# Performance work log

Measured on AMD Instinct MI355X. Metric: run time of the kernel, lower is better.

The kernel has to match this reference:

```python
import jax, jax.numpy as jnp
import numpy as np

B, L, D, H, FF, K = 2, 2048, 512, 16, 2048, 5
HD = D // H
EPS = 1e-5


def _ln(x, g, b):
    m = jnp.mean(x, axis=-1, keepdims=True)
    v = jnp.var(x, axis=-1, keepdims=True)
    return (x - m) / jnp.sqrt(v + EPS) * g + b


def _rope_table(seq_len, hd):
    pos = jnp.arange(seq_len, dtype=jnp.float32)
    inv = 1.0 / (10000.0 ** (jnp.arange(0, hd, 2, dtype=jnp.float32) / hd))
    ang = pos[:, None] * inv[None, :]            # [L, hd/2]
    return jnp.concatenate([jnp.cos(ang), jnp.sin(ang)], axis=-1)  # [L, hd]


def setup_inputs() -> dict:
    key = jax.random.key(0)
    ks = jax.random.split(key, 32)
    w = lambda k, shape: jax.random.normal(k, shape, jnp.float32) * 0.02
    z = lambda n: jnp.zeros((n,), jnp.float32)
    o = lambda n: jnp.ones((n,), jnp.float32)
    return {
        'src': jax.random.normal(ks[0], (B, L, D), jnp.float32),
        'Wq': w(ks[1], (D, D)), 'bq': z(D),
        'Wk': w(ks[2], (D, D)), 'bk': z(D),
        'Wv': w(ks[3], (D, D)), 'bv': z(D),
        'Wo': w(ks[4], (D, D)), 'bo': z(D),
        'ln_g': o(D), 'ln_b': z(D),
        'pw1_w': w(ks[5], (2 * D, D)), 'pw1_b': z(2 * D),
        'dw_w': w(ks[6], (D, 1, K)), 'dw_b': z(D),
        'bn_g': o(D), 'bn_b': z(D),
        'pw2_w': w(ks[7], (D, D)), 'pw2_b': z(D),
        'proj_w': w(ks[8], (L, L)), 'proj_b': z(L),
        'proj2_w': w(ks[9], (D, D)), 'proj2_b': z(D),
        'W1': w(ks[10], (FF, D)), 'b1': z(FF),
        'W2': w(ks[11], (D, FF)), 'b2': z(D),
        'n1_g': o(D), 'n1_b': z(D),
        'n2_g': o(D), 'n2_b': z(D),
    }


def reference(src, Wq, bq, Wk, bk, Wv, bv, Wo, bo, ln_g, ln_b,
              pw1_w, pw1_b, dw_w, dw_b, bn_g, bn_b, pw2_w, pw2_b,
              proj_w, proj_b, proj2_w, proj2_b, W1, b1, W2, b2,
              n1_g, n1_b, n2_g, n2_b):
    scale = HD ** -0.5
    pe = _rope_table(L, HD)
    c, s = pe[:, ::2], pe[:, 1::2]   # faithful to apply_RoPE's interleaved slicing of [cos|sin]

    def rope(x):  # x: [B,H,L,hd]
        xe, xo = x[..., ::2], x[..., 1::2]
        return jnp.concatenate([xe * c - xo * s, xe * s + xo * c], axis=-1)

    q = (src @ Wq.T + bq).reshape(B, L, H, HD).transpose(0, 2, 1, 3)
    k = (src @ Wk.T + bk).reshape(B, L, H, HD).transpose(0, 2, 1, 3)
    v = (src @ Wv.T + bv).reshape(B, L, H, HD).transpose(0, 2, 1, 3)
    q, k = rope(q), rope(k)

    slopes = jnp.asarray(2.0 ** (-(2.0 ** (-(np.log2(H) - 3.0))) * np.arange(H)), jnp.float32)
    idx = jnp.arange(L)
    dist = jnp.clip(idx[:, None] - idx[None, :], 0, None).astype(jnp.float32)
    alibi = slopes[:, None, None] * dist  # [H,L,L]

    scores = jnp.einsum('bhld,bhmd->bhlm', q, k) * scale + alibi[None]
    attn = jax.nn.softmax(scores, axis=-1)
    ctx = jnp.einsum('bhlm,bhmd->bhld', attn, v).transpose(0, 2, 1, 3).reshape(B, L, D)
    attn_out = ctx @ Wo.T + bo

    x0 = src + _ln(attn_out, n1_g, n1_b)

    # depthwise conformer conv block (stride=1, residual downsample = identity)
    x = _ln(x0, ln_g, ln_b)
    x = x @ pw1_w.T + pw1_b                      # [B,L,2D]
    a, g = x[..., :D], x[..., D:]
    x = a * jax.nn.sigmoid(g)                    # GLU
    x = x.transpose(0, 2, 1)                     # [B,D,L]
    x = jax.lax.conv_general_dilated(x, dw_w, (1,), [(K // 2, K // 2)],
                                     dimension_numbers=('NCH', 'OIH', 'NCH'),
                                     feature_group_count=D) + dw_b[None, :, None]
    x = x * (bn_g / jnp.sqrt(1.0 + EPS))[None, :, None] + bn_b[None, :, None]  # BN eval (mu=0, var=1)
    x = x * jnp.clip(x + 3.0, 0.0, 6.0) / 6.0    # hardswish
    conv = x.transpose(0, 2, 1) @ pw2_w.T + pw2_b + x0

    # seq-dim projection branch
    p = jnp.einsum('bld,ml->bmd', x0, proj_w) + proj_b[None, :, None]
    p = p @ proj2_w.T + proj2_b

    y = p + conv
    ff = jax.nn.gelu(y @ W1.T + b1, approximate=False) @ W2.T + b2
    return _ln(y + ff, n2_g, n2_b)
```

## Files before the change

kernel.cpp:

```cpp
#include <hip/hip_runtime.h>
#include <math.h>

#define B_ 2
#define L_ 2048
#define D_ 512
#define H_ 16
#define HD_ 32
#define FF_ 2048
#define BL_ 4096
#define EPS_ 1e-5f

typedef unsigned short ushort;
typedef unsigned int uint;
typedef __attribute__((ext_vector_type(8))) short bf16x8;
typedef __attribute__((ext_vector_type(4))) float f32x4;
typedef __attribute__((ext_vector_type(4))) uint u32x4;

__device__ __forceinline__ ushort bf16r(float f) {
  uint u = __float_as_uint(f);
  uint r = (u + 0x7FFFu + ((u >> 16) & 1u)) >> 16;
  return (ushort)r;
}
__device__ __forceinline__ float bf2f(uint u) { return __uint_as_float(u << 16); }

__device__ __forceinline__ float wsum(float v) {
#pragma unroll
  for (int o = 32; o; o >>= 1) v += __shfl_xor(v, o);
  return v;
}

__device__ __forceinline__ float gelu_fast(float x) {
  float t = x + 0.044715f * x * x * x;
  float e = exp2f(fminf(2.302118131f * t, 80.f));
  return x * e / (1.f + e);
}

__device__ __forceinline__ void gload16(const void* g, void* l) {
  __builtin_amdgcn_global_load_lds(
      (const __attribute__((address_space(1))) void*)g,
      (__attribute__((address_space(3))) void*)l, 16, 0, 0);
}

template <int TMv, int TNv, int EPI, int BROW, int GELU, int RES, int OUTF, int OUTB, int SPK>
__global__ __launch_bounds__(256, 2) void gemm_bf_k(
    const ushort* __restrict__ A, const ushort* __restrict__ W,
    const float* __restrict__ bias, const float* __restrict__ res,
    float* __restrict__ Cf, ushort* __restrict__ Cb,
    const int M, const int N, const int Kd, const long sW, const long sC,
    const int ldC,
    const float* __restrict__ tab, ushort* __restrict__ Qb,
    ushort* __restrict__ Kb, ushort* __restrict__ Vb) {
  constexpr int MF = (TMv == 128) ? 4 : ((TNv == 128) ? 4 : 2);
  constexpr int NF = (TNv == 128) ? ((TMv == 128) ? 4 : 2) : 2;
  __shared__ __align__(16) ushort As[TMv * 64];
  __shared__ __align__(16) ushort Ws[TNv * 64];
  const int tid = threadIdx.x;
  const int wid = tid >> 6, lane = tid & 63;
  const int lane15 = lane & 15, lgrp = lane >> 4;
  const int rowoff = (TMv == 128) ? (wid >> 1) * 64
                                  : ((TNv == 64) ? (wid >> 1) * 32 : 0);
  const int wnoff = (TMv == 128) ? (wid & 1) * 64
                                 : ((TNv == 128) ? wid * 32 : (wid & 1) * 32);
  const int bm = blockIdx.y * TMv, bn = blockIdx.x * TNv;
  const int z = blockIdx.z;
  const int lda = SPK ? (Kd << 1) : Kd;
  const int kh = SPK ? (z & 1) : 0;
  const int zb = SPK ? (z >> 1) : z;
  const ushort* Az = A + (size_t)kh * Kd;
  const ushort* Wz = W + (size_t)zb * sW + (size_t)kh * Kd;

  f32x4 acc[MF][NF];
#pragma unroll
  for (int i = 0; i < MF; ++i)
#pragma unroll
    for (int j = 0; j < NF; ++j) acc[i][j] = (f32x4){0.f, 0.f, 0.f, 0.f};

  for (int k0 = 0; k0 < Kd; k0 += 64) {
    __syncthreads();
#pragma unroll
    for (int i = 0; i < TMv / 32; ++i) {
      const int cb = i * 256 + wid * 64;
      const int chunk = cb + lane;
      const int ml = chunk >> 3;
      const int c16 = (chunk & 7) ^ (ml & 7);
      gload16(Az + (size_t)(bm + ml) * lda + k0 + c16 * 8, &As[(size_t)cb * 8]);
    }
#pragma unroll
    for (int i = 0; i < TNv / 32; ++i) {
      const int cb = i * 256 + wid * 64;
      const int chunk = cb + lane;
      const int ml = chunk >> 3;
      const int c16 = (chunk & 7) ^ (ml & 7);
      gload16(Wz + (size_t)(bn + ml) * lda + k0 + c16 * 8, &Ws[(size_t)cb * 8]);
    }
    __syncthreads();

    bf16x8 af[2][MF], wf[2][NF];
#pragma unroll
    for (int kk = 0; kk < 2; ++kk) {
#pragma unroll
      for (int f = 0; f < MF; ++f) {
        const int ma = rowoff + f * 16 + lane15;
        const int ca = (kk * 4 + lgrp) ^ (ma & 7);
        af[kk][f] = *(const bf16x8*)&As[ma * 64 + ca * 8];
      }
#pragma unroll
      for (int f = 0; f < NF; ++f) {
        const int nb = wnoff + f * 16 + lane15;
        const int cw = (kk * 4 + lgrp) ^ (nb & 7);
        wf[kk][f] = *(const bf16x8*)&Ws[nb * 64 + cw * 8];
      }
    }
#pragma unroll
    for (int kk = 0; kk < 2; ++kk)
#pragma unroll
      for (int fm = 0; fm < MF; ++fm)
#pragma unroll
        for (int fn = 0; fn < NF; ++fn)
          acc[fm][fn] = __builtin_amdgcn_mfma_f32_16x16x32_bf16(
              af[kk][fm], wf[kk][fn], acc[fm][fn], 0, 0, 0);
  }

#pragma unroll
  for (int fm = 0; fm < MF; ++fm) {
#pragma unroll
    for (int fn = 0; fn < NF; ++fn) {
      const int n = bn + wnoff + fn * 16 + lane15;
      float bcol = 0.f;
      if (EPI == 2) bcol = bias[(n >> 1) + (n & 1) * 512];
      else if ((EPI == 1 || !BROW) && bias) bcol = bias[n];
#pragma unroll
      for (int r = 0; r < 4; ++r) {
        const int m = bm + rowoff + fm * 16 + lgrp * 4 + r;
        float val = acc[fm][fn][r];
        if (EPI == 1) {
          val += bcol;
          float p = __shfl_xor(val, 1);
          const int l = m & 2047, b = m >> 11;
          const int h = (n >> 5) & 15;
          if (n < 1024) {
            const int ch = n & 31, i2 = ch >> 1;
            const float cv = tab[l * 32 + i2], sv = tab[l * 32 + 16 + i2];
            const float o = (ch & 1) ? (p * sv + val * cv) : (val * cv - p * sv);
            const int dcol = (ch & 1) ? 16 + i2 : i2;
            if (n < 512)
              Qb[(((size_t)(b * 16 + h)) * 2048 + l) * 32 + dcol] =
                  bf16r(o * (0.1767766952966369f * 1.4426950408889634f));
            else
              Kb[(((size_t)(b * 16 + h)) * 2048 + l) * 32 + dcol] = bf16r(o);
          } else {
            Vb[(((size_t)(b * 16 + h)) * 2048 + l) * 32 + (n & 31)] = bf16r(val);
          }
        } else if (EPI == 2) {
          val += bcol;
          float p = __shfl_xor(val, 1);
          if (!(n & 1)) {
            float glu = val / (1.f + __expf(-p));
            Cb[(size_t)m * 512 + (n >> 1)] = bf16r(glu);
          }
        } else {
          val += BROW ? (bias ? bias[m] : 0.f) : bcol;
          if (RES) val += res[(size_t)m * N + n];
          if (GELU) val = gelu_fast(val);
          const size_t o = (size_t)z * sC + (size_t)m * ldC + n;
          if (OUTF) Cf[o] = val;
          if (OUTB) Cb[o] = bf16r(val);
        }
      }
    }
  }
}

struct CvtArgs {
  const float* s[11];
  ushort* d[11];
  int n[11];
  int pm[11];
};
__global__ __launch_bounds__(256) void cvt_all_k(CvtArgs a) {
  const int seg = blockIdx.y;
  const int n = a.n[seg];
  const int i = (blockIdx.x * 256 + threadIdx.x) * 8;
  if (i >= n) return;
  const float* s = a.s[seg] + i;
  float4 x = *(const float4*)s, y = *(const float4*)(s + 4);
  bf16x8 o;
  o[0] = (short)bf16r(x.x); o[1] = (short)bf16r(x.y);
  o[2] = (short)bf16r(x.z); o[3] = (short)bf16r(x.w);
  o[4] = (short)bf16r(y.x); o[5] = (short)bf16r(y.y);
  o[6] = (short)bf16r(y.z); o[7] = (short)bf16r(y.w);
  ushort* d = a.d[seg] + i;
  const int pm = a.pm[seg];
  if (pm == 1) {
    int cc = i >> 3;
    int row = cc >> 6, off = cc & 63;
    int nrow = (row < 512) ? row * 2 : (row - 512) * 2 + 1;
    d = a.d[seg] + (((size_t)nrow << 6) + off) * 8;
  } else if (pm >= 2) {
    d = a.d[seg] + (size_t)(i >> 9) * 1024 + (i & 511) + ((pm == 3) ? 512 : 0);
  }
  *(bf16x8*)d = o;
}

__global__ void misc_k(float* __restrict__ tab, const float* __restrict__ bq,
                       const float* __restrict__ bk, const float* __restrict__ bv,
                       float* __restrict__ bqkv, const float* __restrict__ p2b,
                       const float* __restrict__ pw2b, float* __restrict__ bcat) {
  if (blockIdx.x < 128) {
    int t = blockIdx.x * 256 + threadIdx.x;
    int i = t & 15, l = t >> 4;
    float cv, sv;
    if (i < 8) {
      float inv0 = 1.0f / powf(10000.0f, (float)(2 * i) / 16.0f);
      float inv1 = 1.0f / powf(10000.0f, (float)(2 * i + 1) / 16.0f);
      cv = cosf((float)l * inv0);
      sv = cosf((float)l * inv1);
    } else {
      int ii = i - 8;
      float inv0 = 1.0f / powf(10000.0f, (float)(2 * ii) / 16.0f);
      float inv1 = 1.0f / powf(10000.0f, (float)(2 * ii + 1) / 16.0f);
      cv = sinf((float)l * inv0);
      sv = sinf((float)l * inv1);
    }
    tab[l * 32 + i] = cv;
    tab[l * 32 + 16 + i] = sv;
  } else {
    int i = threadIdx.x;
    bqkv[i] = bq[i];            bqkv[i + 256] = bq[i + 256];
    bqkv[512 + i] = bk[i];      bqkv[768 + i] = bk[i + 256];
    bqkv[1024 + i] = bv[i];     bqkv[1280 + i] = bv[i + 256];
    bcat[i] = p2b[i] + pw2b[i];
    bcat[i + 256] = p2b[i + 256] + pw2b[i + 256];
  }
}

__global__ __launch_bounds__(256) void transp_k(const float* __restrict__ x,
                                                ushort* __restrict__ xT) {
  __shared__ float t[32][33];
  const int b = blockIdx.z, l0 = blockIdx.x * 32, d0 = blockIdx.y * 32;
  const int tx = threadIdx.x & 31, ty = threadIdx.x >> 5;
#pragma unroll
  for (int i = 0; i < 4; ++i)
    t[ty + i * 8][tx] = x[((size_t)(b * L_ + l0 + ty + i * 8)) * D_ + d0 + tx];
  __syncthreads();
#pragma unroll
  for (int i = 0; i < 4; ++i)
    xT[((size_t)(b * D_ + d0 + ty + i * 8)) * L_ + l0 + tx] =
        bf16r(t[tx][ty + i * 8]);
}

__global__ __launch_bounds__(256) void cmb_proj_k(const ushort* __restrict__ p,
                                                  const float* __restrict__ biasRow,
                                                  ushort* __restrict__ cat) {
  int t = blockIdx.x * 256 + threadIdx.x;
  int n4 = t & 127;
  int m = (t >> 7) & 2047;
  int zb = t >> 18;
  size_t i0 = ((size_t)(zb * 2) * 2048 + m) * 512 + n4 * 4;
  uint2 a = *(const uint2*)&p[i0];
  uint2 b = *(const uint2*)&p[i0 + (size_t)2048 * 512];
  float bm = biasRow[m];
  float o0 = bf2f(a.x & 0xffffu) + bf2f(b.x & 0xffffu) + bm;
  float o1 = bf2f(a.x >> 16) + bf2f(b.x >> 16) + bm;
  float o2 = bf2f(a.y & 0xffffu) + bf2f(b.y & 0xffffu) + bm;
  float o3 = bf2f(a.y >> 16) + bf2f(b.y >> 16) + bm;
  uint lo = (uint)bf16r(o0) | ((uint)bf16r(o1) << 16);
  uint hi = (uint)bf16r(o2) | ((uint)bf16r(o3) << 16);
  uint2 ov = {lo, hi};
  *(uint2*)&cat[((size_t)(zb * 2048 + m)) * 1024 + n4 * 4] = ov;
}

__global__ __launch_bounds__(512, 4) void attn_mfma_k(const ushort* __restrict__ q,
                                                      const ushort* __restrict__ k,
                                                      const ushort* __restrict__ v,
                                                      ushort* __restrict__ ctx) {
  __shared__ __align__(16) ushort K_lds[4][130][8];
  __shared__ __align__(16) uint V_lds[32][68];
  const int tid = threadIdx.x;
  const int wid = tid >> 6, lane = tid & 63;
  const int s = lane >> 4, lr = lane & 15;
  const int bid = blockIdx.x;
  const int xcd = bid & 7, idx = bid >> 3;
  const int bh = xcd * 4 + (idx & 3);
  const int qt = idx >> 2;
  const int qb = qt * 128;
  const int h = bh & 15, bidx = bh >> 4;
  const float nslope = -exp2f(-0.5f * (float)h) * 1.4426950408889634f;
  const int qrow = qb + wid * 16 + lr;
  const float qgf = (float)qrow;
  const float cq = nslope * qgf;
  bf16x8 qa = *(const bf16x8*)&q[((size_t)bh * L_ + qrow) * HD_ + s * 8];

  bf16x8 vones;
#pragma unroll
  for (int i = 0; i < 8; ++i) vones[i] = (short)0x3F80;

  f32x4 acc0 = {0.f, 0.f, 0.f, 0.f}, acc1 = {0.f, 0.f, 0.f, 0.f};
  f32x4 accl = {0.f, 0.f, 0.f, 0.f};
  const ushort* kg = k + (size_t)bh * L_ * HD_;
  const ushort* vg = v + (size_t)bh * L_ * HD_;
  const int vslot = (lane & 48) + ((lane >> 1) & 3) * 4 + ((lane >> 3) & 1) * 2 + (lane & 1);
  const int kkey = tid >> 2, kslot = tid & 3;

  bf16x8 kreg;
  uint2 va, vb;
  {
    kreg = *(const bf16x8*)&kg[(size_t)kkey * HD_ + kslot * 8];
    const ushort* g0 = vg + (size_t)(2 * lane) * HD_ + wid * 4;
    va = *(const uint2*)g0;
    vb = *(const uint2*)(g0 + HD_);
  }

  for (int t0 = 0; t0 < L_; t0 += 128) {
    __syncthreads();
    *(bf16x8*)&K_lds[kslot][kkey][0] = kreg;
    V_lds[wid * 4 + 0][vslot] = __builtin_amdgcn_perm(vb.x, va.x, 0x05040100u);
    V_lds[wid * 4 + 1][vslot] = __builtin_amdgcn_perm(vb.x, va.x, 0x07060302u);
    V_lds[wid * 4 + 2][vslot] = __builtin_amdgcn_perm(vb.y, va.y, 0x05040100u);
    V_lds[wid * 4 + 3][vslot] = __builtin_amdgcn_perm(vb.y, va.y, 0x07060302u);
    if (t0 + 128 < L_) {
      kreg = *(const bf16x8*)&kg[(size_t)(t0 + 128 + kkey) * HD_ + kslot * 8];
      const ushort* g0 = vg + (size_t)(t0 + 128 + 2 * lane) * HD_ + wid * 4;
      va = *(const uint2*)g0;
      vb = *(const uint2*)(g0 + HD_);
    }
    asm volatile("s_waitcnt lgkmcnt(0)" ::: "memory");
    __builtin_amdgcn_s_barrier();
    __builtin_amdgcn_sched_barrier(0);

    f32x4 sc[8];
    __builtin_amdgcn_s_setprio(1);
#pragma unroll
    for (int c = 0; c < 8; ++c) {
      bf16x8 kf = *(const bf16x8*)&K_lds[s][c * 16 + lr][0];
      f32x4 zz = {0.f, 0.f, 0.f, 0.f};
      sc[c] = __builtin_amdgcn_mfma_f32_16x16x32_bf16(kf, qa, zz, 0, 0, 0);
    }
    __builtin_amdgcn_s_setprio(0);
    if (t0 < qb) {
      const float kb0 = (float)(t0 + s * 4);
#pragma unroll
      for (int c = 0; c < 8; ++c) {
        const float kc = kb0 + (float)(c * 16);
#pragma unroll
        for (int r = 0; r < 4; ++r)
          sc[c][r] = exp2f(fmaf(nslope, kc + (float)r, sc[c][r]));
      }
    } else if (t0 > qb) {
#pragma unroll
      for (int c = 0; c < 8; ++c)
#pragma unroll
        for (int r = 0; r < 4; ++r) sc[c][r] = exp2f(sc[c][r] + cq);
    } else {
      const float kb0 = (float)(t0 + s * 4);
#pragma unroll
      for (int c = 0; c < 8; ++c) {
        const float kc = kb0 + (float)(c * 16);
#pragma unroll
        for (int r = 0; r < 4; ++r) {
          float mn = fminf(kc + (float)r, qgf);
          sc[c][r] = exp2f(fmaf(nslope, mn, sc[c][r]));
        }
      }
    }
#pragma unroll
    for (int t = 0; t < 4; ++t) {
      uint w0 = __builtin_amdgcn_perm(__float_as_uint(sc[2 * t][1]),
                                      __float_as_uint(sc[2 * t][0]), 0x07060302u);
      uint w1 = __builtin_amdgcn_perm(__float_as_uint(sc[2 * t][3]),
                                      __float_as_uint(sc[2 * t][2]), 0x07060302u);
      uint w2 = __builtin_amdgcn_perm(__float_as_uint(sc[2 * t + 1][1]),
                                      __float_as_uint(sc[2 * t + 1][0]), 0x07060302u);
      uint w3 = __builtin_amdgcn_perm(__float_as_uint(sc[2 * t + 1][3]),
                                      __float_as_uint(sc[2 * t + 1][2]), 0x07060302u);
      u32x4 pw = {w0, w1, w2, w3};
      bf16x8 pf = __builtin_bit_cast(bf16x8, pw);
      bf16x8 v0 = *(const bf16x8*)&V_lds[lr][t * 16 + s * 4];
      bf16x8 v1 = *(const bf16x8*)&V_lds[16 + lr][t * 16 + s * 4];
      __builtin_amdgcn_s_setprio(1);
      acc0 = __builtin_amdgcn_mfma_f32_16x16x32_bf16(pf, v0, acc0, 0, 0, 0);
      acc1 = __builtin_amdgcn_mfma_f32_16x16x32_bf16(pf, v1, acc1, 0, 0, 0);
      accl = __builtin_amdgcn_mfma_f32_16x16x32_bf16(pf, vones, accl, 0, 0, 0);
      __builtin_amdgcn_s_setprio(0);
    }
  }
#pragma unroll
  for (int r = 0; r < 4; ++r) {
    float il = 1.f / accl[r];
    int qg2 = qb + wid * 16 + s * 4 + r;
    ushort* op = ctx + ((size_t)(bidx * L_ + qg2)) * D_ + h * HD_;
    op[lr] = bf16r(acc0[r] * il);
    op[16 + lr] = bf16r(acc1[r] * il);
  }
}

__global__ __launch_bounds__(64) void ln_res_ln_k(
    const float* __restrict__ x, const float* __restrict__ res,
    const float* __restrict__ g1, const float* __restrict__ b1,
    const float* __restrict__ g2, const float* __restrict__ b2,
    float* __restrict__ x0, ushort* __restrict__ xln) {
  int row = blockIdx.x, lane = threadIdx.x;
  const float* xr = x + (size_t)row * D_;
  float v[8];
  float s = 0.f, ss = 0.f;
#pragma unroll
  for (int i = 0; i < 8; ++i) {
    float t = xr[i * 64 + lane];
    v[i] = t; s += t; ss += t * t;
  }
  s = wsum(s); ss = wsum(ss);
  float mean = s * (1.f / 512.f);
  float rstd = rsqrtf(ss * (1.f / 512.f) - mean * mean + EPS_);
  float w[8];
  float s2 = 0.f, ss2 = 0.f;
#pragma unroll
  for (int i = 0; i < 8; ++i) {
    int idx = i * 64 + lane;
    float t = res[(size_t)row * D_ + idx] + (v[i] - mean) * rstd * g1[idx] + b1[idx];
    w[i] = t; s2 += t; ss2 += t * t;
  }
  s2 = wsum(s2); ss2 = wsum(ss2);
  float mean2 = s2 * (1.f / 512.f);
  float rstd2 = rsqrtf(ss2 * (1.f / 512.f) - mean2 * mean2 + EPS_);
#pragma unroll
  for (int i = 0; i < 8; ++i) {
    int idx = i * 64 + lane;
    x0[(size_t)row * D_ + idx] = w[i];
    xln[(size_t)row * D_ + idx] = bf16r((w[i] - mean2) * rstd2 * g2[idx] + b2[idx]);
  }
}

__global__ __launch_bounds__(64) void ln2_k(const float* __restrict__ zA,
                                            const float* __restrict__ zB,
                                            const float* __restrict__ yres,
                                            const float* __restrict__ b2,
                                            const float* __restrict__ g,
                                            const float* __restrict__ bb,
                                            float* __restrict__ out) {
  int row = blockIdx.x, lane = threadIdx.x;
  const size_t base = (size_t)row * D_;
  float v[8];
  float s = 0.f, ss = 0.f;
#pragma unroll
  for (int i = 0; i < 8; ++i) {
    int idx = i * 64 + lane;
    float t = zA[base + idx] + zB[base + idx] + b2[idx] + yres[base + idx];
    v[i] = t; s += t; ss += t * t;
  }
  s = wsum(s); ss = wsum(ss);
  float mean = s * (1.f / 512.f);
  float rstd = rsqrtf(ss * (1.f / 512.f) - mean * mean + EPS_);
#pragma unroll
  for (int i = 0; i < 8; ++i) {
    int idx = i * 64 + lane;
    out[base + idx] = (v[i] - mean) * rstd * g[idx] + bb[idx];
  }
}

__global__ __launch_bounds__(256) void convbn_k(
    const ushort* __restrict__ x, const float* __restrict__ w,
    const float* __restrict__ wb, const float* __restrict__ bng,
    const float* __restrict__ bnb, ushort* __restrict__ out) {
  int t = blockIdx.x * 256 + threadIdx.x;
  int c4 = t & 127;
  int l = (t >> 7) & 2047;
  int b = t >> 18;
  int d0 = c4 * 4;
  float accv[4] = {0.f, 0.f, 0.f, 0.f};
#pragma unroll
  for (int kt = 0; kt < 5; ++kt) {
    int ls = l + kt - 2;
    if (ls >= 0 && ls < L_) {
      uint2 xv = *(const uint2*)&x[((size_t)(b * L_ + ls)) * D_ + d0];
      float pv[4] = {bf2f(xv.x & 0xffffu), bf2f(xv.x >> 16),
                     bf2f(xv.y & 0xffffu), bf2f(xv.y >> 16)};
#pragma unroll
      for (int j = 0; j < 4; ++j) accv[j] += pv[j] * w[(d0 + j) * 5 + kt];
    }
  }
  const float bscale = rsqrtf(1.0f + EPS_);
  float po[4];
#pragma unroll
  for (int j = 0; j < 4; ++j) {
    int d = d0 + j;
    float vv = accv[j] + wb[d];
    vv = vv * (bng[d] * bscale) + bnb[d];
    float hs = fminf(fmaxf(vv + 3.f, 0.f), 6.f);
    po[j] = vv * hs * (1.f / 6.f);
  }
  uint lo = (uint)bf16r(po[0]) | ((uint)bf16r(po[1]) << 16);
  uint hi = (uint)bf16r(po[2]) | ((uint)bf16r(po[3]) << 16);
  uint2 o2 = {lo, hi};
  *(uint2*)&out[((size_t)(b * L_ + l)) * 1024 + d0] = o2;
}

extern "C" void kernel_launch(void* const* d_in, const int* in_sizes, int n_in,
                              void* d_out, int out_size, void* d_ws, size_t ws_size,
                              hipStream_t stream) {
  const float* src    = (const float*)d_in[0];
  const float* Wq     = (const float*)d_in[1];
  const float* bq     = (const float*)d_in[2];
  const float* Wk     = (const float*)d_in[3];
  const float* bk     = (const float*)d_in[4];
  const float* Wv     = (const float*)d_in[5];
  const float* bv     = (const float*)d_in[6];
  const float* Wo     = (const float*)d_in[7];
  const float* bo     = (const float*)d_in[8];
  const float* ln_g   = (const float*)d_in[9];
  const float* ln_b   = (const float*)d_in[10];
  const float* pw1_w  = (const float*)d_in[11];
  const float* pw1_b  = (const float*)d_in[12];
  const float* dw_w   = (const float*)d_in[13];
  const float* dw_b   = (const float*)d_in[14];
  const float* bn_g   = (const float*)d_in[15];
  const float* bn_b   = (const float*)d_in[16];
  const float* pw2_w  = (const float*)d_in[17];
  const float* pw2_b  = (const float*)d_in[18];
  const float* proj_w = (const float*)d_in[19];
  const float* proj_b = (const float*)d_in[20];
  const float* proj2_w= (const float*)d_in[21];
  const float* proj2_b= (const float*)d_in[22];
  const float* W1     = (const float*)d_in[23];
  const float* b1     = (const float*)d_in[24];
  const float* W2     = (const float*)d_in[25];
  const float* b2     = (const float*)d_in[26];
  const float* n1_g   = (const float*)d_in[27];
  const float* n1_b   = (const float*)d_in[28];
  const float* n2_g   = (const float*)d_in[29];
  const float* n2_b   = (const float*)d_in[30];
  float* out = (float*)d_out;

  char* wsb = (char*)d_ws;
  const size_t MB1 = 1 << 20;
  ushort* wqkv = (ushort*)(wsb);
  ushort* wo_w = (ushort*)(wsb + 1536 * 1024);
  ushort* pw1w = (ushort*)(wsb + 2 * MB1);
  ushort* wcat = (ushort*)(wsb + 3 * MB1);
  ushort* pjww = (ushort*)(wsb + 4 * MB1);
  ushort* w1w  = (ushort*)(wsb + 12 * MB1);
  ushort* w2w  = (ushort*)(wsb + 14 * MB1);
  float*  bqkv = (float*)(wsb + 16 * MB1);
  float*  bcat = (float*)(wsb + 16 * MB1 + 6144);
  float*  tab  = (float*)(wsb + 16 * MB1 + 8192);
  char* A0 = wsb + 17 * MB1;
  ushort* src_bf = (ushort*)A0;
  ushort* pprt   = (ushort*)A0;
  ushort* ff_bf  = (ushort*)A0;
  float*  x0     = (float*)(A0 + 8 * MB1);
  char* B0 = A0 + 16 * MB1;
  ushort* Qb = (ushort*)B0;
  ushort* Kb = (ushort*)(B0 + 4 * MB1);
  ushort* Vb = (ushort*)(B0 + 8 * MB1);
  ushort* glu_bf = (ushort*)B0;
  ushort* xln_bf = (ushort*)(B0 + 8 * MB1);
  ushort* cat_bf = (ushort*)(B0 + 4 * MB1);
  float*  zprt   = (float*)B0;
  char* C0 = B0 + 12 * MB1;
  ushort* ctx_bf = (ushort*)C0;
  ushort* x0T    = (ushort*)C0;
  ushort* y_bf   = (ushort*)C0;
  char* D0 = C0 + 4 * MB1;
  float* attnout = (float*)D0;
  float* y       = (float*)D0;

  dim3 blk(256);

  CvtArgs ca;
  for (int i = 0; i < 11; ++i) ca.pm[i] = 0;
  ca.s[0] = Wq;     ca.d[0] = wqkv;              ca.n[0] = 512 * 512;
  ca.s[1] = Wk;     ca.d[1] = wqkv + 512 * 512;  ca.n[1] = 512 * 512;
  ca.s[2] = Wv;     ca.d[2] = wqkv + 1024 * 512; ca.n[2] = 512 * 512;
  ca.s[3] = Wo;     ca.d[3] = wo_w;              ca.n[3] = 512 * 512;
  ca.s[4] = pw1_w;  ca.d[4] = pw1w;              ca.n[4] = 1024 * 512; ca.pm[4] = 1;
  ca.s[5] = pw2_w;  ca.d[5] = wcat;              ca.n[5] = 512 * 512;  ca.pm[5] = 3;
  ca.s[6] = proj_w; ca.d[6] = pjww;              ca.n[6] = 2048 * 2048;
  ca.s[7] = proj2_w;ca.d[7] = wcat;              ca.n[7] = 512 * 512;  ca.pm[7] = 2;
  ca.s[8] = W1;     ca.d[8] = w1w;               ca.n[8] = 2048 * 512;
  ca.s[9] = W2;     ca.d[9] = w2w;               ca.n[9] = 512 * 2048;
  ca.s[10]= src;    ca.d[10]= src_bf;            ca.n[10]= BL_ * D_;
  cvt_all_k<<<dim3(2048, 11), blk, 0, stream>>>(ca);
  misc_k<<<dim3(129), blk, 0, stream>>>(tab, bq, bk, bv, bqkv, proj2_b, pw2_b, bcat);

  gemm_bf_k<64,128,1,0,0,0,0,0,0><<<dim3(12, 64), blk, 0, stream>>>(
      src_bf, wqkv, bqkv, nullptr, nullptr, nullptr,
      BL_, 1536, 512, 0, 0, 1536, tab, Qb, Kb, Vb);

  attn_mfma_k<<<dim3(512), dim3(512), 0, stream>>>(Qb, Kb, Vb, ctx_bf);

  gemm_bf_k<64,64,0,0,0,0,1,0,0><<<dim3(8, 64), blk, 0, stream>>>(
      ctx_bf, wo_w, bo, nullptr, attnout, nullptr,
      BL_, 512, 512, 0, 0, 512, nullptr, nullptr, nullptr, nullptr);

  ln_res_ln_k<<<BL_, 64, 0, stream>>>(attnout, src, n1_g, n1_b, ln_g, ln_b,
                                      x0, xln_bf);

  transp_k<<<dim3(64, 16, 2), blk, 0, stream>>>(x0, x0T);

  gemm_bf_k<64,128,2,0,0,0,0,1,0><<<dim3(8, 64), blk, 0, stream>>>(
      xln_bf, pw1w, pw1_b, nullptr, nullptr, glu_bf,
      BL_, 1024, 512, 0, 0, 512, nullptr, nullptr, nullptr, nullptr);

  convbn_k<<<(B_ * L_ * (D_ / 4)) / 256, blk, 0, stream>>>(
      glu_bf, dw_w, dw_b, bn_g, bn_b, cat_bf + 512);

  gemm_bf_k<64,64,0,0,0,0,0,1,1><<<dim3(8, 32, 4), blk, 0, stream>>>(
      pjww, x0T, nullptr, nullptr, nullptr, pprt,
      2048, 512, 1024, (long)512 * 2048, (long)2048 * 512, 512,
      nullptr, nullptr, nullptr, nullptr);
  cmb_proj_k<<<dim3(2048), blk, 0, stream>>>(pprt, proj_b, cat_bf);

  gemm_bf_k<64,64,0,0,0,1,1,1,0><<<dim3(8, 64), blk, 0, stream>>>(
      cat_bf, wcat, bcat, x0, y, y_bf,
      BL_, 512, 1024, 0, 0, 512, nullptr, nullptr, nullptr, nullptr);

  gemm_bf_k<64,128,0,0,1,0,0,1,0><<<dim3(16, 64), blk, 0, stream>>>(
      y_bf, w1w, b1, nullptr, nullptr, ff_bf,
      BL_, 2048, 512, 0, 0, 2048, nullptr, nullptr, nullptr, nullptr);

  gemm_bf_k<64,64,0,0,0,0,1,0,1><<<dim3(8, 64, 2), blk, 0, stream>>>(
      ff_bf, w2w, nullptr, nullptr, zprt, nullptr,
      BL_, 512, 1024, 0, (long)BL_ * 512, 512,
      nullptr, nullptr, nullptr, nullptr);

  ln2_k<<<BL_, 64, 0, stream>>>(zprt, zprt + (size_t)BL_ * 512, y, b2,
                                n2_g, n2_b, out);
}
```

Before: 220.2 us.

## Split attention key range in two and combine partial sums in new kernel

The attention kernel now splits the 2048-key loop into two halves handled by separate blocks, doubling the grid from 512 to 1024 blocks. Each block writes unnormalized fp32 partial accumulators and row sums to workspace, and a new combine kernel adds the halves, normalizes and writes the bf16 context. The aim is better occupancy across the GPU's compute units. The cost is an extra launch and roughly 16MB of fp32 partial writes and reads. This is safe without max rescaling because the softmax appears to use a fixed bias rather than a running max.

```diff
diff --git a/kernel.cpp b/kernel.cpp
--- a/kernel.cpp
+++ b/kernel.cpp
@@ -273,18 +273,20 @@
 __global__ __launch_bounds__(512, 4) void attn_mfma_k(const ushort* __restrict__ q,
                                                       const ushort* __restrict__ k,
                                                       const ushort* __restrict__ v,
-                                                      ushort* __restrict__ ctx) {
+                                                      float* __restrict__ pacc,
+                                                      float* __restrict__ plsum) {
   __shared__ __align__(16) ushort K_lds[4][130][8];
   __shared__ __align__(16) uint V_lds[32][68];
   const int tid = threadIdx.x;
   const int wid = tid >> 6, lane = tid & 63;
   const int s = lane >> 4, lr = lane & 15;
   const int bid = blockIdx.x;
-  const int xcd = bid & 7, idx = bid >> 3;
-  const int bh = xcd * 4 + (idx & 3);
-  const int qt = idx >> 2;
+  const int xcd = bid & 7, j = bid >> 3;
+  const int bh = xcd * 4 + (j & 3);
+  const int rest = j >> 2;
+  const int qt = rest >> 1, kh = rest & 1;
   const int qb = qt * 128;
-  const int h = bh & 15, bidx = bh >> 4;
+  const int h = bh & 15;
   const float nslope = -exp2f(-0.5f * (float)h) * 1.4426950408889634f;
   const int qrow = qb + wid * 16 + lr;
   const float qgf = (float)qrow;
@@ -301,24 +303,25 @@
   const ushort* vg = v + (size_t)bh * L_ * HD_;
   const int vslot = (lane & 48) + ((lane >> 1) & 3) * 4 + ((lane >> 3) & 1) * 2 + (lane & 1);
   const int kkey = tid >> 2, kslot = tid & 3;
+  const int tbeg = kh * 1024, tend = tbeg + 1024;
 
   bf16x8 kreg;
   uint2 va, vb;
   {
-    kreg = *(const bf16x8*)&kg[(size_t)kkey * HD_ + kslot * 8];
-    const ushort* g0 = vg + (size_t)(2 * lane) * HD_ + wid * 4;
+    kreg = *(const bf16x8*)&kg[(size_t)(tbeg + kkey) * HD_ + kslot * 8];
+    const ushort* g0 = vg + (size_t)(tbeg + 2 * lane) * HD_ + wid * 4;
     va = *(const uint2*)g0;
     vb = *(const uint2*)(g0 + HD_);
   }
 
-  for (int t0 = 0; t0 < L_; t0 += 128) {
+  for (int t0 = tbeg; t0 < tend; t0 += 128) {
     __syncthreads();
     *(bf16x8*)&K_lds[kslot][kkey][0] = kreg;
     V_lds[wid * 4 + 0][vslot] = __builtin_amdgcn_perm(vb.x, va.x, 0x05040100u);
     V_lds[wid * 4 + 1][vslot] = __builtin_amdgcn_perm(vb.x, va.x, 0x07060302u);
     V_lds[wid * 4 + 2][vslot] = __builtin_amdgcn_perm(vb.y, va.y, 0x05040100u);
     V_lds[wid * 4 + 3][vslot] = __builtin_amdgcn_perm(vb.y, va.y, 0x07060302u);
-    if (t0 + 128 < L_) {
+    if (t0 + 128 < tend) {
       kreg = *(const bf16x8*)&kg[(size_t)(t0 + 128 + kkey) * HD_ + kslot * 8];
       const ushort* g0 = vg + (size_t)(t0 + 128 + 2 * lane) * HD_ + wid * 4;
       va = *(const uint2*)g0;
@@ -384,14 +387,41 @@
       __builtin_amdgcn_s_setprio(0);
     }
   }
+  const size_t pbase = (size_t)bid * 4096;
 #pragma unroll
   for (int r = 0; r < 4; ++r) {
-    float il = 1.f / accl[r];
-    int qg2 = qb + wid * 16 + s * 4 + r;
-    ushort* op = ctx + ((size_t)(bidx * L_ + qg2)) * D_ + h * HD_;
-    op[lr] = bf16r(acc0[r] * il);
-    op[16 + lr] = bf16r(acc1[r] * il);
-  }
+    int qloc = wid * 16 + s * 4 + r;
+    pacc[pbase + qloc * 32 + lr] = acc0[r];
+    pacc[pbase + qloc * 32 + 16 + lr] = acc1[r];
+  }
+  if (lr == 0) {
+#pragma unroll
+    for (int r = 0; r < 4; ++r)
+      plsum[bid * 128 + wid * 16 + s * 4 + r] = accl[r];
+  }
+}
+
+__global__ __launch_bounds__(256) void cmb_attn_k(const float* __restrict__ pacc,
+                                                  const float* __restrict__ plsum,
+                                                  ushort* __restrict__ ctx) {
+  int t = blockIdx.x * 256 + threadIdx.x;
+  int cg = t & 3, qloc = (t >> 2) & 127, qt = (t >> 9) & 15, bh = t >> 13;
+  int bidA = ((qt * 2 * 4) + (bh & 3)) * 8 + (bh >> 2);
+  int bidB = bidA + 32;
+  size_t iA = (size_t)bidA * 4096 + qloc * 32 + cg * 8;
+  size_t iB = (size_t)bidB * 4096 + qloc * 32 + cg * 8;
+  f32x4 a0 = *(const f32x4*)&pacc[iA];
+  f32x4 a1 = *(const f32x4*)&pacc[iA + 4];
+  f32x4 b0 = *(const f32x4*)&pacc[iB];
+  f32x4 b1 = *(const f32x4*)&pacc[iB + 4];
+  float il = 1.f / (plsum[bidA * 128 + qloc] + plsum[bidB * 128 + qloc]);
+  int qg = qt * 128 + qloc, h = bh & 15, bidx = bh >> 4;
+  uint o0 = (uint)bf16r((a0[0] + b0[0]) * il) | ((uint)bf16r((a0[1] + b0[1]) * il) << 16);
+  uint o1 = (uint)bf16r((a0[2] + b0[2]) * il) | ((uint)bf16r((a0[3] + b0[3]) * il) << 16);
+  uint o2 = (uint)bf16r((a1[0] + b1[0]) * il) | ((uint)bf16r((a1[1] + b1[1]) * il) << 16);
+  uint o3 = (uint)bf16r((a1[2] + b1[2]) * il) | ((uint)bf16r((a1[3] + b1[3]) * il) << 16);
+  u32x4 ov = {o0, o1, o2, o3};
+  *(u32x4*)&ctx[((size_t)(bidx * L_ + qg)) * D_ + h * HD_ + cg * 8] = ov;
 }
 
 __global__ __launch_bounds__(64) void ln_res_ln_k(
@@ -544,6 +574,7 @@
   float*  tab  = (float*)(wsb + 16 * MB1 + 8192);
   char* A0 = wsb + 17 * MB1;
   ushort* src_bf = (ushort*)A0;
+  float*  pacc   = (float*)A0;
   ushort* pprt   = (ushort*)A0;
   ushort* ff_bf  = (ushort*)A0;
   float*  x0     = (float*)(A0 + 8 * MB1);
@@ -560,6 +591,7 @@
   ushort* x0T    = (ushort*)C0;
   ushort* y_bf   = (ushort*)C0;
   char* D0 = C0 + 4 * MB1;
+  float* plsum   = (float*)D0;
   float* attnout = (float*)D0;
   float* y       = (float*)D0;
 
@@ -585,7 +617,8 @@
       src_bf, wqkv, bqkv, nullptr, nullptr, nullptr,
       BL_, 1536, 512, 0, 0, 1536, tab, Qb, Kb, Vb);
 
-  attn_mfma_k<<<dim3(512), dim3(512), 0, stream>>>(Qb, Kb, Vb, ctx_bf);
+  attn_mfma_k<<<dim3(1024), dim3(512), 0, stream>>>(Qb, Kb, Vb, pacc, plsum);
+  cmb_attn_k<<<dim3(1024), blk, 0, stream>>>(pacc, plsum, ctx_bf);
 
   gemm_bf_k<64,64,0,0,0,0,1,0,0><<<dim3(8, 64), blk, 0, stream>>>(
       ctx_bf, wo_w, bo, nullptr, attnout, nullptr,
```

Result: slower. 224.6 us (+2.0%).
